# Kernel tuning notes

Hardware: AMD Instinct MI355X
Metric: run time of the kernel (lower is better)

Reference implementation:

```python
import jax, jax.numpy as jnp
import numpy as np

B, N, C, H = 8, 1024, 768, 12
D = C // H  # head_dim = 64
SCALE = D ** -0.5


def setup_inputs() -> dict:
    key = jax.random.key(0)
    ks = jax.random.split(key, 5)
    s = lambda k, sh, fan: jax.random.normal(k, sh, jnp.float32) * (fan ** -0.5)
    return {
        "x": jax.random.normal(ks[0], (B, N, C), jnp.float32),
        "w_qkv": s(ks[1], (C, 3 * C), C),
        "b_qkv": jnp.zeros((3 * C,), jnp.float32),
        "w_l": s(ks[2], (H, H), H),
        "b_l": jnp.zeros((H,), jnp.float32),
        "w_w": s(ks[3], (H, H), H),
        "b_w": jnp.zeros((H,), jnp.float32),
        "w_proj": s(ks[4], (C, C), C),
        "b_proj": jnp.zeros((C,), jnp.float32),
    }


def reference(x, w_qkv, b_qkv, w_l, b_l, w_w, b_w, w_proj, b_proj):
    Bq, Nq, Cq = x.shape
    # qkv projection -> (3, B, H, N, D)
    qkv = (x @ w_qkv + b_qkv).reshape(Bq, Nq, 3, H, D).transpose(2, 0, 3, 1, 4)
    q, k, v = qkv[0] * SCALE, qkv[1], qkv[2]
    # raw scores [B, H, N, N]
    attn = jnp.einsum("bhnd,bhmd->bhnm", q, k)
    # pre-softmax talking-heads: mix across head axis (Dense over H)
    attn = jnp.einsum("bhnm,hg->bgnm", attn, w_l) + b_l[None, :, None, None]
    attn = jax.nn.softmax(attn, axis=-1)
    # post-softmax talking-heads
    attn = jnp.einsum("bhnm,hg->bgnm", attn, w_w) + b_w[None, :, None, None]
    # weighted values -> (B, N, C)
    out = jnp.einsum("bhnm,bhmd->bnhd", attn, v).reshape(Bq, Nq, Cq)
    return out @ w_proj + b_proj
```

## Files before the change

kernel.cpp:

```cpp
#include <hip/hip_runtime.h>

#define BB 8
#define NN 1024
#define CC 768
#define HH 12
#define DD 64

typedef unsigned short u16;
typedef unsigned int u32;
typedef __attribute__((ext_vector_type(8))) short s16x8;
typedef __attribute__((ext_vector_type(4))) short s16x4;
typedef __attribute__((ext_vector_type(4))) float f32x4;
typedef __attribute__((ext_vector_type(2))) u32 u32x2;
typedef __attribute__((ext_vector_type(4))) u32 u32x4;

__device__ __forceinline__ float bf2f(u16 u) {
  u32 x = ((u32)u) << 16;
  return __builtin_bit_cast(float, x);
}
__device__ __forceinline__ u16 f2bf(float f) {
  u32 x = __builtin_bit_cast(u32, f);
  x += 0x7fffu + ((x >> 16) & 1u);
  return (u16)(x >> 16);
}
__device__ __forceinline__ float hw_exp2(float x) { return __builtin_amdgcn_exp2f(x); }
__device__ __forceinline__ float hw_log2(float x) { return __builtin_amdgcn_logf(x); }
__device__ __forceinline__ s16x8 lds_read8(const u16* p) {
  u32x2 a = *(const u32x2*)p;
  u32x2 b = *(const u32x2*)(p + 4);
  u32x4 m = {a.x, a.y, b.x, b.y};
  return __builtin_bit_cast(s16x8, m);
}
__device__ __forceinline__ u32 packhl(float v) {
  u32 xv = __builtin_bit_cast(u32, v);
  float lo = v - __builtin_bit_cast(float, xv & 0xFFFF0000u);
  return (xv >> 16) | (__builtin_bit_cast(u32, lo) & 0xFFFF0000u);
}
__device__ __forceinline__ void gload_lds16(const u16* g, u16* l) {
  __builtin_amdgcn_global_load_lds(
      (const __attribute__((address_space(1))) u32*)g,
      (__attribute__((address_space(3))) u32*)l, 16, 0, 0);
}

__global__ __launch_bounds__(256) void convx_kernel(const float* __restrict__ in,
                                                    u16* __restrict__ out) {
  size_t i = ((size_t)blockIdx.x * 256 + threadIdx.x) * 8;
  f32x4 a = *(const f32x4*)(in + i);
  f32x4 b = *(const f32x4*)(in + i + 4);
  s16x8 r;
#pragma unroll
  for (int j = 0; j < 4; j++) { r[j] = (short)f2bf(a[j]); r[4 + j] = (short)f2bf(b[j]); }
  *(s16x8*)(out + i) = r;
}

__global__ __launch_bounds__(256) void transpose_kernel(const float* __restrict__ in,
                                                        u16* __restrict__ out,
                                                        int R, int C) {
  __shared__ float t[32][33];
  const int cl = threadIdx.x & 31, rq = threadIdx.x >> 5;
#pragma unroll
  for (int rr = 0; rr < 4; rr++) {
    int rl = rq * 4 + rr;
    t[rl][cl] = in[(size_t)(blockIdx.y * 32 + rl) * C + blockIdx.x * 32 + cl];
  }
  __syncthreads();
#pragma unroll
  for (int rr = 0; rr < 4; rr++) {
    int oc = rq * 4 + rr;
    out[(size_t)(blockIdx.x * 32 + oc) * R + blockIdx.y * 32 + cl] = f2bf(t[cl][oc]);
  }
}

__global__ __launch_bounds__(256) void qkv_gemm(
    const u16* __restrict__ A, const u16* __restrict__ Bt, const float* __restrict__ bias,
    u16* __restrict__ qo, u16* __restrict__ ko, u16* __restrict__ vo) {
  __shared__ __align__(16) u16 As[128 * 32];
  __shared__ __align__(16) u16 Bs[128 * 32];
  const int tid = threadIdx.x;
  const int w = tid >> 6, lane = tid & 63, l15 = lane & 15, l4 = lane >> 4;
  const int wm = w & 1, wn = w >> 1;
  const int m0 = blockIdx.x * 128, n0 = blockIdx.y * 128;
  const int grow = lane >> 2, gcol = (lane & 3) * 8;

  f32x4 acc[4][4];
#pragma unroll
  for (int a = 0; a < 4; a++)
#pragma unroll
    for (int bb = 0; bb < 4; bb++) acc[a][bb] = (f32x4){0.f, 0.f, 0.f, 0.f};

  for (int k0 = 0; k0 < CC; k0 += 32) {
    __syncthreads();
    const u16* ga = A + (size_t)(m0 + w * 32 + grow) * CC + k0 + gcol;
    const u16* gb = Bt + (size_t)(n0 + w * 32 + grow) * CC + k0 + gcol;
    gload_lds16(ga, &As[w * 1024]);
    gload_lds16(ga + (size_t)16 * CC, &As[w * 1024 + 512]);
    gload_lds16(gb, &Bs[w * 1024]);
    gload_lds16(gb + (size_t)16 * CC, &Bs[w * 1024 + 512]);
    __syncthreads();
    s16x8 af[4], bf[4];
#pragma unroll
    for (int a = 0; a < 4; a++) af[a] = *(const s16x8*)&As[(wm * 64 + a * 16 + l15) * 32 + l4 * 8];
#pragma unroll
    for (int bb = 0; bb < 4; bb++) bf[bb] = *(const s16x8*)&Bs[(wn * 64 + bb * 16 + l15) * 32 + l4 * 8];
#pragma unroll
    for (int a = 0; a < 4; a++)
#pragma unroll
      for (int bb = 0; bb < 4; bb++)
        acc[a][bb] = __builtin_amdgcn_mfma_f32_16x16x32_bf16(af[a], bf[bb], acc[a][bb], 0, 0, 0);
  }

  const int b = (m0 >> 10);
#pragma unroll
  for (int bb = 0; bb < 4; bb++) {
    int col = n0 + wn * 64 + bb * 16 + l15;
    int s = col / CC;
    int rem = col - s * CC;
    int h = rem >> 6, d = rem & 63;
    float bv = bias[col];
#pragma unroll
    for (int a = 0; a < 4; a++) {
      int row0 = m0 + wm * 64 + a * 16 + l4 * 4;
      int nt0 = row0 & (NN - 1);
      if (s == 2) {
        s16x4 pk;
#pragma unroll
        for (int r = 0; r < 4; r++) pk[r] = (short)f2bf(acc[a][bb][r] + bv);
        *(s16x4*)(vo + (((size_t)((b * HH + h) * DD + d)) << 10) + nt0) = pk;
      } else if (s == 0) {
#pragma unroll
        for (int r = 0; r < 4; r++)
          qo[(((size_t)((b * HH + h) * NN + nt0 + r)) << 6) + d] = f2bf((acc[a][bb][r] + bv) * 0.125f);
      } else {
#pragma unroll
        for (int r = 0; r < 4; r++)
          ko[(((size_t)((b * HH + h) * NN + nt0 + r)) << 6) + d] = f2bf(acc[a][bb][r] + bv);
      }
    }
  }
}

__global__ __launch_bounds__(256) void proj_gemm(
    const u16* __restrict__ A, const u16* __restrict__ Bt, const float* __restrict__ bias,
    float* __restrict__ out) {
  __shared__ __align__(16) u16 As[128 * 32];
  __shared__ __align__(16) u16 Bs[128 * 32];
  const int tid = threadIdx.x;
  const int w = tid >> 6, lane = tid & 63, l15 = lane & 15, l4 = lane >> 4;
  const int wm = w & 1, wn = w >> 1;
  const int m0 = blockIdx.x * 128, n0 = blockIdx.y * 128;
  const int grow = lane >> 2, gcol = (lane & 3) * 8;

  f32x4 acc[4][4];
#pragma unroll
  for (int a = 0; a < 4; a++)
#pragma unroll
    for (int bb = 0; bb < 4; bb++) acc[a][bb] = (f32x4){0.f, 0.f, 0.f, 0.f};

  for (int k0 = 0; k0 < CC; k0 += 32) {
    __syncthreads();
    const u16* ga = A + (size_t)(m0 + w * 32 + grow) * CC + k0 + gcol;
    const u16* gb = Bt + (size_t)(n0 + w * 32 + grow) * CC + k0 + gcol;
    gload_lds16(ga, &As[w * 1024]);
    gload_lds16(ga + (size_t)16 * CC, &As[w * 1024 + 512]);
    gload_lds16(gb, &Bs[w * 1024]);
    gload_lds16(gb + (size_t)16 * CC, &Bs[w * 1024 + 512]);
    __syncthreads();
    s16x8 af[4], bf[4];
#pragma unroll
    for (int a = 0; a < 4; a++) af[a] = *(const s16x8*)&As[(wm * 64 + a * 16 + l15) * 32 + l4 * 8];
#pragma unroll
    for (int bb = 0; bb < 4; bb++) bf[bb] = *(const s16x8*)&Bs[(wn * 64 + bb * 16 + l15) * 32 + l4 * 8];
#pragma unroll
    for (int a = 0; a < 4; a++)
#pragma unroll
      for (int bb = 0; bb < 4; bb++)
        acc[a][bb] = __builtin_amdgcn_mfma_f32_16x16x32_bf16(af[a], bf[bb], acc[a][bb], 0, 0, 0);
  }

#pragma unroll
  for (int bb = 0; bb < 4; bb++) {
    int col = n0 + wn * 64 + bb * 16 + l15;
    float bv = bias[col];
#pragma unroll
    for (int a = 0; a < 4; a++) {
      int row0 = m0 + wm * 64 + a * 16 + l4 * 4;
#pragma unroll
      for (int r = 0; r < 4; r++)
        out[(size_t)(row0 + r) * CC + col] = acc[a][bb][r] + bv;
    }
  }
}

#define SB_BYTES 28736
#define UT_OFF   SB_BYTES
#define UT_ELE   6912
#define LL2_OFF  (SB_BYTES + 27648)
#define SM_TOTAL (LL2_OFF + 1088)

__global__ __launch_bounds__(512, 4) void attn_kernel(
    const u16* __restrict__ qg, const u16* __restrict__ kg, const u16* __restrict__ vtg,
    const float* __restrict__ wlg, const float* __restrict__ blg,
    const float* __restrict__ wwg, const float* __restrict__ bwg,
    u16* __restrict__ aout) {
  __shared__ __align__(16) char smem[SM_TOTAL];
  u16* Sb = (u16*)smem;
  u16* Ut0 = (u16*)(smem + UT_OFF);
  float* lpart = (float*)(smem + UT_OFF);
  float* ll2 = (float*)(smem + LL2_OFF);

  const int b = blockIdx.x, i0 = blockIdx.y * 16;
  const int tid = threadIdx.x;
  const int w = tid >> 6, lane = tid & 63, l15 = lane & 15, l4 = lane >> 4;
  const float RLN2 = 1.44269504088896340736f;

  for (int j = tid; j < SB_BYTES / 4; j += 512) ((u32*)smem)[j] = 0;
  __syncthreads();

  s16x8 wlS, wlA1, wlA2, wwA1, wwA2;
#pragma unroll
  for (int j = 0; j < 8; j++) {
    int k = l4 * 8 + j;
    float v1 = (k < 12 && l15 < 12) ? wlg[k * 12 + l15] * RLN2 : 0.f;
    wlS[j] = (short)f2bf(v1);
    int h = k >> 1, pt = k & 1;
    float v2 = (h < 12 && l15 < 12) ? wlg[h * 12 + l15] * RLN2 : 0.f;
    u16 h2 = f2bf(v2); u16 lo2 = f2bf(v2 - bf2f(h2));
    wlA1[j] = (short)h2; wlA2[j] = (short)(pt ? 0 : lo2);
    float v3 = (h < 12 && l15 < 12) ? wwg[h * 12 + l15] : 0.f;
    u16 h3 = f2bf(v3); u16 lo3 = f2bf(v3 - bf2f(h3));
    wwA1[j] = (short)h3; wwA2[j] = (short)(pt ? 0 : lo3);
  }
  int gr[4]; float blv[4], bwv[4];
#pragma unroll
  for (int r = 0; r < 4; r++) {
    gr[r] = l4 * 4 + r;
    blv[r] = (gr[r] < 12) ? blg[gr[r]] * RLN2 : 0.f;
    bwv[r] = (gr[r] < 12) ? bwg[gr[r]] : 0.f;
  }

  int jh[3], jmb[3];
  s16x8 qf[3][2];
#pragma unroll
  for (int jt = 0; jt < 3; jt++) {
    int j = w * 3 + jt;
    jh[jt] = j % 12; jmb[jt] = j / 12;
    const u16* qp = qg + (((size_t)((b * HH + jh[jt]) * NN + i0 + l15)) << 6) + l4 * 8;
    qf[jt][0] = *(const s16x8*)qp;
    qf[jt][1] = *(const s16x8*)(qp + 32);
  }

  float la[4] = {0.f, 0.f, 0.f, 0.f};
  for (int mt = 0; mt < 32; mt++) {
    const int m0 = mt * 32;
#pragma unroll
    for (int jt = 0; jt < 3; jt++) {
      const u16* kp = kg + (((size_t)((b * HH + jh[jt]) * NN + m0 + jmb[jt] * 16 + l15)) << 6) + l4 * 8;
      f32x4 ca = (f32x4){0.f, 0.f, 0.f, 0.f};
      f32x4 cb = (f32x4){0.f, 0.f, 0.f, 0.f};
      ca = __builtin_amdgcn_mfma_f32_16x16x32_bf16(*(const s16x8*)kp, qf[jt][0], ca, 0, 0, 0);
      cb = __builtin_amdgcn_mfma_f32_16x16x32_bf16(*(const s16x8*)(kp + 32), qf[jt][1], cb, 0, 0, 0);
      f32x4 c = ca + cb;
      int cbse = (jmb[jt] * 16 + l4 * 4) * 16 + l15;
#pragma unroll
      for (int r = 0; r < 4; r++)
        Sb[(size_t)(cbse + r * 16) * 20 + jh[jt]] = f2bf(c[r]);
    }
    __syncthreads();
#pragma unroll
    for (int tt = 0; tt < 4; tt++) {
      int t = w * 4 + tt;
      s16x8 bS = lds_read8(Sb + (size_t)(t * 16 + l15) * 20 + l4 * 8);
      f32x4 T = (f32x4){blv[0], blv[1], blv[2], blv[3]};
      T = __builtin_amdgcn_mfma_f32_16x16x32_bf16(wlS, bS, T, 0, 0, 0);
#pragma unroll
      for (int r = 0; r < 4; r++) la[r] += hw_exp2(T[r]);
    }
    __syncthreads();
  }

#pragma unroll
  for (int r = 0; r < 4; r++) lpart[w * 256 + gr[r] * 16 + l15] = la[r];
  __syncthreads();
  if (tid < 256) {
    float s = 0.f;
#pragma unroll
    for (int w2 = 0; w2 < 8; w2++) s += lpart[w2 * 256 + tid];
    ll2[(tid >> 4) * 17 + (tid & 15)] = hw_log2(s);
  }
  __syncthreads();
  float Tinit[4];
#pragma unroll
  for (int r = 0; r < 4; r++) Tinit[r] = blv[r] - ll2[gr[r] * 17 + l15];

  const int db = w >> 1, pvh = (w & 1) * 6;
  f32x4 O[6];
#pragma unroll
  for (int jp = 0; jp < 6; jp++) O[jp] = (f32x4){0.f, 0.f, 0.f, 0.f};

  for (int mt = 0; mt < 32; mt++) {
    const int m0 = mt * 32;
    u16* Utb = Ut0 + (mt & 1) * UT_ELE;
#pragma unroll
    for (int jt = 0; jt < 3; jt++) {
      const u16* kp = kg + (((size_t)((b * HH + jh[jt]) * NN + m0 + jmb[jt] * 16 + l15)) << 6) + l4 * 8;
      f32x4 ca = (f32x4){0.f, 0.f, 0.f, 0.f};
      f32x4 cb = (f32x4){0.f, 0.f, 0.f, 0.f};
      ca = __builtin_amdgcn_mfma_f32_16x16x32_bf16(*(const s16x8*)kp, qf[jt][0], ca, 0, 0, 0);
      cb = __builtin_amdgcn_mfma_f32_16x16x32_bf16(*(const s16x8*)(kp + 32), qf[jt][1], cb, 0, 0, 0);
      f32x4 c = ca + cb;
      int cbse = (jmb[jt] * 16 + l4 * 4) * 16 + l15;
#pragma unroll
      for (int r = 0; r < 4; r++)
        *(u32*)(Sb + (size_t)(cbse + r * 16) * 28 + 2 * jh[jt]) = packhl(c[r]);
    }
    __syncthreads();
#pragma unroll
    for (int tt = 0; tt < 4; tt++) {
      int t = w * 4 + tt;
      s16x8 bS = lds_read8(Sb + (size_t)(t * 16 + l15) * 28 + l4 * 8);
      f32x4 Ta = (f32x4){Tinit[0], Tinit[1], Tinit[2], Tinit[3]};
      f32x4 Tb = (f32x4){0.f, 0.f, 0.f, 0.f};
      Ta = __builtin_amdgcn_mfma_f32_16x16x32_bf16(wlA1, bS, Ta, 0, 0, 0);
      Tb = __builtin_amdgcn_mfma_f32_16x16x32_bf16(wlA2, bS, Tb, 0, 0, 0);
      f32x4 T = Ta + Tb;
      u32x4 pk;
#pragma unroll
      for (int r = 0; r < 4; r++) pk[r] = packhl(hw_exp2(T[r]));
      s16x8 bP = __builtin_bit_cast(s16x8, pk);
      f32x4 Ua = (f32x4){bwv[0], bwv[1], bwv[2], bwv[3]};
      f32x4 Ub = (f32x4){0.f, 0.f, 0.f, 0.f};
      Ua = __builtin_amdgcn_mfma_f32_16x16x32_bf16(wwA1, bP, Ua, 0, 0, 0);
      Ub = __builtin_amdgcn_mfma_f32_16x16x32_bf16(wwA2, bP, Ub, 0, 0, 0);
      f32x4 U = Ua + Ub;
#pragma unroll
      for (int r = 0; r < 4; r++)
        if (gr[r] < 12) Utb[(size_t)(gr[r] * 16 + l15) * 36 + t] = f2bf(U[r]);
    }
    __syncthreads();
#pragma unroll
    for (int jp = 0; jp < 6; jp++) {
      const int h = pvh + jp;
      s16x8 aV = *(const s16x8*)(vtg + (((size_t)((b * HH + h) * DD + db * 16 + l15)) << 10) + m0 + l4 * 8);
      s16x8 bU = lds_read8(Utb + (size_t)(h * 16 + l15) * 36 + l4 * 8);
      O[jp] = __builtin_amdgcn_mfma_f32_16x16x32_bf16(aV, bU, O[jp], 0, 0, 0);
    }
  }

#pragma unroll
  for (int jp = 0; jp < 6; jp++) {
    const int h = pvh + jp;
    const int d0 = db * 16 + l4 * 4;
    s16x4 pk4;
#pragma unroll
    for (int r = 0; r < 4; r++) pk4[r] = (short)f2bf(O[jp][r]);
    *(s16x4*)(aout + ((size_t)(b * NN) + i0 + l15) * CC + h * DD + d0) = pk4;
  }
}

extern "C" void kernel_launch(void* const* d_in, const int* in_sizes, int n_in,
                              void* d_out, int out_size, void* d_ws, size_t ws_size,
                              hipStream_t stream) {
  const float* x      = (const float*)d_in[0];
  const float* w_qkv  = (const float*)d_in[1];
  const float* b_qkv  = (const float*)d_in[2];
  const float* w_l    = (const float*)d_in[3];
  const float* b_l    = (const float*)d_in[4];
  const float* w_w    = (const float*)d_in[5];
  const float* b_w    = (const float*)d_in[6];
  const float* w_proj = (const float*)d_in[7];
  const float* b_proj = (const float*)d_in[8];

  const size_t per = (size_t)BB * HH * NN * DD;
  u16* xb  = (u16*)d_ws;
  u16* wqt = xb + per;
  u16* wpt = wqt + (size_t)3 * CC * CC;
  u16* q   = wpt + (size_t)CC * CC;
  u16* k   = q + per;
  u16* vt  = k + per;
  u16* ao  = vt + per;

  convx_kernel<<<3072, 256, 0, stream>>>(x, xb);
  transpose_kernel<<<dim3(3 * CC / 32, CC / 32), 256, 0, stream>>>(w_qkv, wqt, CC, 3 * CC);
  transpose_kernel<<<dim3(CC / 32, CC / 32), 256, 0, stream>>>(w_proj, wpt, CC, CC);
  qkv_gemm<<<dim3(64, 18), 256, 0, stream>>>(xb, wqt, b_qkv, q, k, vt);
  attn_kernel<<<dim3(BB, NN / 16), 512, 0, stream>>>(q, k, vt, w_l, b_l, w_w, b_w, ao);
  proj_gemm<<<dim3(64, 6), 256, 0, stream>>>(ao, wpt, b_proj, (float*)d_out);
}
```

Before: 449.0 us.

## Double-buffer LDS tiles in QKV and projection GEMMs to overlap loads with MFMA

Both GEMM kernels now use two LDS buffers per operand. The next K-slice is issued with global-to-LDS loads before computing on the current one, synchronised by explicit vmcnt waits and barriers. This hides global load latency behind the MFMA work instead of serialising load then compute each iteration. The cost is double the LDS per block, which may lower occupancy, and manual waitcnt handling that relies on the per-thread load count being exactly four.

Result: no change. 446.0 us (-0.7%).

```diff
diff --git a/kernel.cpp b/kernel.cpp
--- a/kernel.cpp
+++ b/kernel.cpp
@@ -74,39 +74,54 @@
 __global__ __launch_bounds__(256) void qkv_gemm(
     const u16* __restrict__ A, const u16* __restrict__ Bt, const float* __restrict__ bias,
     u16* __restrict__ qo, u16* __restrict__ ko, u16* __restrict__ vo) {
-  __shared__ __align__(16) u16 As[128 * 32];
-  __shared__ __align__(16) u16 Bs[128 * 32];
+  __shared__ __align__(16) u16 As[2][128 * 32];
+  __shared__ __align__(16) u16 Bs[2][128 * 32];
   const int tid = threadIdx.x;
   const int w = tid >> 6, lane = tid & 63, l15 = lane & 15, l4 = lane >> 4;
   const int wm = w & 1, wn = w >> 1;
   const int m0 = blockIdx.x * 128, n0 = blockIdx.y * 128;
   const int grow = lane >> 2, gcol = (lane & 3) * 8;
 
+  const u16* ga0 = A + (size_t)(m0 + w * 32 + grow) * CC + gcol;
+  const u16* gb0 = Bt + (size_t)(n0 + w * 32 + grow) * CC + gcol;
+
   f32x4 acc[4][4];
 #pragma unroll
   for (int a = 0; a < 4; a++)
 #pragma unroll
     for (int bb = 0; bb < 4; bb++) acc[a][bb] = (f32x4){0.f, 0.f, 0.f, 0.f};
 
-  for (int k0 = 0; k0 < CC; k0 += 32) {
-    __syncthreads();
-    const u16* ga = A + (size_t)(m0 + w * 32 + grow) * CC + k0 + gcol;
-    const u16* gb = Bt + (size_t)(n0 + w * 32 + grow) * CC + k0 + gcol;
-    gload_lds16(ga, &As[w * 1024]);
-    gload_lds16(ga + (size_t)16 * CC, &As[w * 1024 + 512]);
-    gload_lds16(gb, &Bs[w * 1024]);
-    gload_lds16(gb + (size_t)16 * CC, &Bs[w * 1024 + 512]);
-    __syncthreads();
+  gload_lds16(ga0, &As[0][w * 1024]);
+  gload_lds16(ga0 + (size_t)16 * CC, &As[0][w * 1024 + 512]);
+  gload_lds16(gb0, &Bs[0][w * 1024]);
+  gload_lds16(gb0 + (size_t)16 * CC, &Bs[0][w * 1024 + 512]);
+
+  for (int t = 0; t < 24; ++t) {
+    const int cb = t & 1, nb = cb ^ 1;
+    if (t + 1 < 24) {
+      const u16* ga = ga0 + (t + 1) * 32;
+      const u16* gb = gb0 + (t + 1) * 32;
+      gload_lds16(ga, &As[nb][w * 1024]);
+      gload_lds16(ga + (size_t)16 * CC, &As[nb][w * 1024 + 512]);
+      gload_lds16(gb, &Bs[nb][w * 1024]);
+      gload_lds16(gb + (size_t)16 * CC, &Bs[nb][w * 1024 + 512]);
+      asm volatile("s_waitcnt vmcnt(4)" ::: "memory");
+    } else {
+      asm volatile("s_waitcnt vmcnt(0)" ::: "memory");
+    }
+    __builtin_amdgcn_s_barrier();
     s16x8 af[4], bf[4];
 #pragma unroll
-    for (int a = 0; a < 4; a++) af[a] = *(const s16x8*)&As[(wm * 64 + a * 16 + l15) * 32 + l4 * 8];
-#pragma unroll
-    for (int bb = 0; bb < 4; bb++) bf[bb] = *(const s16x8*)&Bs[(wn * 64 + bb * 16 + l15) * 32 + l4 * 8];
+    for (int a = 0; a < 4; a++) af[a] = *(const s16x8*)&As[cb][(wm * 64 + a * 16 + l15) * 32 + l4 * 8];
+#pragma unroll
+    for (int bb = 0; bb < 4; bb++) bf[bb] = *(const s16x8*)&Bs[cb][(wn * 64 + bb * 16 + l15) * 32 + l4 * 8];
 #pragma unroll
     for (int a = 0; a < 4; a++)
 #pragma unroll
       for (int bb = 0; bb < 4; bb++)
         acc[a][bb] = __builtin_amdgcn_mfma_f32_16x16x32_bf16(af[a], bf[bb], acc[a][bb], 0, 0, 0);
+    asm volatile("s_waitcnt lgkmcnt(0)" ::: "memory");
+    __builtin_amdgcn_s_barrier();
   }
 
   const int b = (m0 >> 10);
@@ -142,39 +157,54 @@
 __global__ __launch_bounds__(256) void proj_gemm(
     const u16* __restrict__ A, const u16* __restrict__ Bt, const float* __restrict__ bias,
     float* __restrict__ out) {
-  __shared__ __align__(16) u16 As[128 * 32];
-  __shared__ __align__(16) u16 Bs[128 * 32];
+  __shared__ __align__(16) u16 As[2][128 * 32];
+  __shared__ __align__(16) u16 Bs[2][128 * 32];
   const int tid = threadIdx.x;
   const int w = tid >> 6, lane = tid & 63, l15 = lane & 15, l4 = lane >> 4;
   const int wm = w & 1, wn = w >> 1;
   const int m0 = blockIdx.x * 128, n0 = blockIdx.y * 128;
   const int grow = lane >> 2, gcol = (lane & 3) * 8;
 
+  const u16* ga0 = A + (size_t)(m0 + w * 32 + grow) * CC + gcol;
+  const u16* gb0 = Bt + (size_t)(n0 + w * 32 + grow) * CC + gcol;
+
   f32x4 acc[4][4];
 #pragma unroll
   for (int a = 0; a < 4; a++)
 #pragma unroll
     for (int bb = 0; bb < 4; bb++) acc[a][bb] = (f32x4){0.f, 0.f, 0.f, 0.f};
 
-  for (int k0 = 0; k0 < CC; k0 += 32) {
-    __syncthreads();
-    const u16* ga = A + (size_t)(m0 + w * 32 + grow) * CC + k0 + gcol;
-    const u16* gb = Bt + (size_t)(n0 + w * 32 + grow) * CC + k0 + gcol;
-    gload_lds16(ga, &As[w * 1024]);
-    gload_lds16(ga + (size_t)16 * CC, &As[w * 1024 + 512]);
-    gload_lds16(gb, &Bs[w * 1024]);
-    gload_lds16(gb + (size_t)16 * CC, &Bs[w * 1024 + 512]);
-    __syncthreads();
+  gload_lds16(ga0, &As[0][w * 1024]);
+  gload_lds16(ga0 + (size_t)16 * CC, &As[0][w * 1024 + 512]);
+  gload_lds16(gb0, &Bs[0][w * 1024]);
+  gload_lds16(gb0 + (size_t)16 * CC, &Bs[0][w * 1024 + 512]);
+
+  for (int t = 0; t < 24; ++t) {
+    const int cb = t & 1, nb = cb ^ 1;
+    if (t + 1 < 24) {
+      const u16* ga = ga0 + (t + 1) * 32;
+      const u16* gb = gb0 + (t + 1) * 32;
+      gload_lds16(ga, &As[nb][w * 1024]);
+      gload_lds16(ga + (size_t)16 * CC, &As[nb][w * 1024 + 512]);
+      gload_lds16(gb, &Bs[nb][w * 1024]);
+      gload_lds16(gb + (size_t)16 * CC, &Bs[nb][w * 1024 + 512]);
+      asm volatile("s_waitcnt vmcnt(4)" ::: "memory");
+    } else {
+      asm volatile("s_waitcnt vmcnt(0)" ::: "memory");
+    }
+    __builtin_amdgcn_s_barrier();
     s16x8 af[4], bf[4];
 #pragma unroll
-    for (int a = 0; a < 4; a++) af[a] = *(const s16x8*)&As[(wm * 64 + a * 16 + l15) * 32 + l4 * 8];
-#pragma unroll
-    for (int bb = 0; bb < 4; bb++) bf[bb] = *(const s16x8*)&Bs[(wn * 64 + bb * 16 + l15) * 32 + l4 * 8];
+    for (int a = 0; a < 4; a++) af[a] = *(const s16x8*)&As[cb][(wm * 64 + a * 16 + l15) * 32 + l4 * 8];
+#pragma unroll
+    for (int bb = 0; bb < 4; bb++) bf[bb] = *(const s16x8*)&Bs[cb][(wn * 64 + bb * 16 + l15) * 32 + l4 * 8];
 #pragma unroll
     for (int a = 0; a < 4; a++)
 #pragma unroll
       for (int bb = 0; bb < 4; bb++)
         acc[a][bb] = __builtin_amdgcn_mfma_f32_16x16x32_bf16(af[a], bf[bb], acc[a][bb], 0, 0, 0);
+    asm volatile("s_waitcnt lgkmcnt(0)" ::: "memory");
+    __builtin_amdgcn_s_barrier();
   }
 
 #pragma unroll
```
